# Kernel tuning notes

Hardware: AMD Instinct MI355X
Metric: run time of the kernel (lower is better)

The kernel has to match this reference:

```python
import jax, jax.numpy as jnp
import numpy as np

N = 50000
E = 800000
D_IN = 128
H = 128
K = 64
BN_EPS = 1e-5


def setup_inputs() -> dict:
    key = jax.random.key(0)
    ks = jax.random.split(key, 16)
    s_in = 1.0 / np.sqrt(D_IN)
    s_h = 1.0 / np.sqrt(H)
    inp = {
        "x": jax.random.normal(ks[0], (N, D_IN), dtype=jnp.float32),
        "edge_index": jax.random.randint(ks[1], (2, E), 0, N, dtype=jnp.int64),
        # GIN layer 1 MLP (Linear(D_IN,H) -> ReLU -> Linear(H,H)), eps1, BN1
        "W1a": jax.random.uniform(ks[2], (D_IN, H), jnp.float32, -s_in, s_in),
        "b1a": jnp.zeros((H,), jnp.float32),
        "W1b": jax.random.uniform(ks[3], (H, H), jnp.float32, -s_h, s_h),
        "b1b": jnp.zeros((H,), jnp.float32),
        "eps1": jnp.zeros((), jnp.float32),
        "gamma1": jnp.ones((H,), jnp.float32),
        "beta1": jnp.zeros((H,), jnp.float32),
        # GIN layer 2 MLP, eps2, BN2
        "W2a": jax.random.uniform(ks[4], (H, H), jnp.float32, -s_h, s_h),
        "b2a": jnp.zeros((H,), jnp.float32),
        "W2b": jax.random.uniform(ks[5], (H, H), jnp.float32, -s_h, s_h),
        "b2b": jnp.zeros((H,), jnp.float32),
        "eps2": jnp.zeros((), jnp.float32),
        "gamma2": jnp.ones((H,), jnp.float32),
        "beta2": jnp.zeros((H,), jnp.float32),
        # final projection (no bias) and learnable log temperature
        "Wout": jax.random.uniform(ks[6], (H, K), jnp.float32, -s_h, s_h),
        "log_tau": jnp.zeros((), jnp.float32),  # log(1.0)
    }
    return inp


def _gin_layer(x, src, dst, Wa, ba, Wb, bb, eps):
    # GINConv: mlp((1+eps)*x + sum_{j in N(i)} x_j), scatter-add over edges
    agg = jax.ops.segment_sum(x[src], dst, num_segments=N)  # [N, d]
    h = (1.0 + eps) * x + agg
    h = jax.nn.relu(h @ Wa + ba) @ Wb + bb
    return h


def _batchnorm(x, gamma, beta):
    # training-mode BatchNorm1d over node dim (biased variance)
    m = jnp.mean(x, axis=0)
    v = jnp.mean(jnp.square(x - m), axis=0)
    return (x - m) * jax.lax.rsqrt(v + BN_EPS) * gamma + beta


def reference(x, edge_index, W1a, b1a, W1b, b1b, eps1, gamma1, beta1,
              W2a, b2a, W2b, b2b, eps2, gamma2, beta2, Wout, log_tau):
    src, dst = edge_index[0], edge_index[1]
    h = _gin_layer(x, src, dst, W1a, b1a, W1b, b1b, eps1)
    h = jax.nn.relu(_batchnorm(h, gamma1, beta1))
    h = _gin_layer(h, src, dst, W2a, b2a, W2b, b2b, eps2)
    h = jax.nn.relu(_batchnorm(h, gamma2, beta2))
    logits = h @ Wout  # [N, K]
    tau = jnp.exp(log_tau)
    S = jax.nn.softmax(logits / tau, axis=-1)
    return (S, logits)
```

## Files before the change

### kernel.cpp

```cpp
#include <hip/hip_runtime.h>
#include <hip/hip_fp16.h>


#define NNODES 50000
#define NEDGES 800000
#define HD 128
#define KOUT 64
#define NCLS 8
#define CLSW 6250
#define HIST_BLKS 512

typedef __attribute__((ext_vector_type(8))) _Float16 f16x8;
typedef __attribute__((ext_vector_type(4))) float f32x4;

__device__ __forceinline__ unsigned short f2h_bits(float f) {
    _Float16 h = (_Float16)f;
    return __builtin_bit_cast(unsigned short, h);
}
__device__ __forceinline__ f16x8 h8_relu(f16x8 v) {
    #pragma unroll
    for (int i = 0; i < 8; ++i) v[i] = (v[i] > (_Float16)0.f) ? v[i] : (_Float16)0.f;
    return v;
}

__global__ __launch_bounds__(256) void prep_all(
    const float* __restrict__ x, unsigned short* __restrict__ xh,
    const float* __restrict__ W1a, const float* __restrict__ W1b,
    const float* __restrict__ W2a, const float* __restrict__ W2b,
    unsigned short* __restrict__ wt1a, unsigned short* __restrict__ wt1b,
    unsigned short* __restrict__ wt2a, unsigned short* __restrict__ wt2b,
    const int* __restrict__ ei, int* __restrict__ deg)
{
    __shared__ int h[CLSW];
    int bid = blockIdx.x;
    if (bid < HIST_BLKS) {
        const int cls = bid & 7;
        const int lo = cls * CLSW;
        const int e0 = (bid >> 3) * 12500;
        for (int i = threadIdx.x; i < CLSW; i += 256) h[i] = 0;
        __syncthreads();
        for (int e = e0 + threadIdx.x; e < e0 + 12500; e += 256) {
            unsigned d = (unsigned)(ei[NEDGES + e] - lo);
            if (d < (unsigned)CLSW) atomicAdd(&h[d], 1);
        }
        __syncthreads();
        for (int i = threadIdx.x; i < CLSW; i += 256) {
            int v = h[i];
            if (v) atomicAdd(&deg[lo + i], v);
        }
    } else if (bid < HIST_BLKS + 6250) {
        int i = (bid - HIST_BLKS) * 256 + threadIdx.x;
        float4 v = ((const float4*)x)[i];
        ushort4 o;
        o.x = f2h_bits(v.x); o.y = f2h_bits(v.y);
        o.z = f2h_bits(v.z); o.w = f2h_bits(v.w);
        ((ushort4*)xh)[i] = o;
    } else {
        int wb = bid - (HIST_BLKS + 6250);
        int w = wb >> 6;
        int idx = (wb & 63) * 256 + threadIdx.x;
        int n = idx >> 7, k = idx & 127;
        const float* W = (w == 0) ? W1a : (w == 1) ? W1b : (w == 2) ? W2a : W2b;
        unsigned short* Wt = (w == 0) ? wt1a : (w == 1) ? wt1b : (w == 2) ? wt2a : wt2b;
        Wt[idx] = f2h_bits(W[k * HD + n]);
    }
}

__global__ __launch_bounds__(256) void scan_a(
    const int* __restrict__ deg, int* __restrict__ incl, int* __restrict__ bsum)
{
    __shared__ int s[256];
    int t = threadIdx.x, idx = blockIdx.x * 256 + t;
    int v = (idx < NNODES) ? deg[idx] : 0;
    s[t] = v; __syncthreads();
    #pragma unroll
    for (int off = 1; off < 256; off <<= 1) {
        int tmp = (t >= off) ? s[t - off] : 0;
        __syncthreads();
        s[t] += tmp;
        __syncthreads();
    }
    if (idx < NNODES) incl[idx] = s[t];
    if (t == 255) bsum[blockIdx.x] = s[255];
}

__global__ __launch_bounds__(256) void scan_b(
    const int* __restrict__ bsum, int* __restrict__ bscan, int nblk)
{
    __shared__ int s[256];
    int t = threadIdx.x;
    s[t] = (t < nblk) ? bsum[t] : 0; __syncthreads();
    #pragma unroll
    for (int off = 1; off < 256; off <<= 1) {
        int tmp = (t >= off) ? s[t - off] : 0;
        __syncthreads();
        s[t] += tmp;
        __syncthreads();
    }
    bscan[t] = s[t];
}

__global__ __launch_bounds__(256) void scan_c(
    const int* __restrict__ deg, const int* __restrict__ incl,
    const int* __restrict__ bscan,
    int* __restrict__ row_start, int* __restrict__ cur)
{
    int b = blockIdx.x, t = threadIdx.x, idx = b * 256 + t;
    if (idx >= NNODES) return;
    int off = (b > 0) ? bscan[b - 1] : 0;
    int ex = incl[idx] - deg[idx] + off;
    row_start[idx] = ex;
    cur[idx] = ex;
}

__global__ __launch_bounds__(256) void edge_fill(
    const int* __restrict__ ei, int* __restrict__ cur, int* __restrict__ col)
{
    const int cls = blockIdx.x & 7;
    const int e0 = (blockIdx.x >> 3) * 3125;
    for (int e = e0 + threadIdx.x; e < e0 + 3125; e += 256) {
        int dst = ei[NEDGES + e];
        if (dst / CLSW == cls) {
            int pos = atomicAdd(&cur[dst], 1);
            col[pos] = ei[e];
        }
    }
}

template<bool BN>
__global__ __launch_bounds__(256) void gin_gather_w(
    const unsigned short* __restrict__ Xh, const int* __restrict__ col,
    const int* __restrict__ rs, const int* __restrict__ re,
    const float* __restrict__ eps,
    const float* __restrict__ scale, const float* __restrict__ shift,
    unsigned short* __restrict__ H0h)
{
    const int t = threadIdx.x;
    const int g = t >> 4;
    const int lane = t & 15;
    const f16x8* X8 = (const f16x8*)Xh;
    const float alphaf = 1.f + eps[0];

    f16x8 sc8, sh8, al8;
    #pragma unroll
    for (int i = 0; i < 8; ++i) al8[i] = (_Float16)alphaf;
    if (BN) {
        #pragma unroll
        for (int i = 0; i < 8; ++i) {
            sc8[i] = (_Float16)scale[lane * 8 + i];
            sh8[i] = (_Float16)shift[lane * 8 + i];
        }
    }

    #pragma unroll 1
    for (int nn = 0; nn < 2; ++nn) {
        int node = blockIdx.x * 32 + nn * 16 + g;
        if (node >= NNODES) continue;

        f16x8 acc = X8[(long)node * 16 + lane];
        if (BN) acc = h8_relu(acc * sc8 + sh8);
        acc = acc * al8;

        int j = rs[node], end = re[node];
        for (; j + 3 < end; j += 4) {
            f16x8 u0 = X8[(long)col[j]     * 16 + lane];
            f16x8 u1 = X8[(long)col[j + 1] * 16 + lane];
            f16x8 u2 = X8[(long)col[j + 2] * 16 + lane];
            f16x8 u3 = X8[(long)col[j + 3] * 16 + lane];
            if (BN) {
                u0 = h8_relu(u0 * sc8 + sh8);
                u1 = h8_relu(u1 * sc8 + sh8);
                u2 = h8_relu(u2 * sc8 + sh8);
                u3 = h8_relu(u3 * sc8 + sh8);
            }
            acc += (u0 + u1) + (u2 + u3);
        }
        for (; j < end; ++j) {
            f16x8 u = X8[(long)col[j] * 16 + lane];
            if (BN) u = h8_relu(u * sc8 + sh8);
            acc += u;
        }

        ((f16x8*)H0h)[(long)node * 16 + lane] = acc;
    }
}

__global__ __launch_bounds__(256) void mlp_mfma(
    const unsigned short* __restrict__ A,
    const unsigned short* __restrict__ Wta,
    const float* __restrict__ biasa,
    const unsigned short* __restrict__ Wtb,
    const float* __restrict__ biasb,
    unsigned short* __restrict__ Cb,
    float* __restrict__ Cf,
    float* __restrict__ out_sum, float* __restrict__ out_sq)
{
    __shared__ _Float16 Wsa[128][136];
    __shared__ _Float16 Wsb[128][136];
    float (*Cs)[132] = (float(*)[132]) & Wsa[0][0];
    float* redp = (float*)&Wsb[0][0];

    const int t = threadIdx.x;
    const int wave = t >> 6, lane = t & 63;
    const int m16 = lane & 15, quad = lane >> 4;
    const int row0 = blockIdx.x * 64;
    const int arow = row0 + wave * 16 + m16;

    #pragma unroll
    for (int i = 0; i < 8; ++i) {
        int idx = t + i * 256;
        int r = idx >> 4, s = idx & 15;
        *(float4*)&Wsa[r][s * 8] = ((const float4*)Wta)[idx];
        *(float4*)&Wsb[r][s * 8] = ((const float4*)Wtb)[idx];
    }

    f16x8 afrag[4];
    if (arow < NNODES) {
        const _Float16* ar = (const _Float16*)A + (long)arow * HD + quad * 8;
        #pragma unroll
        for (int kc = 0; kc < 4; ++kc)
            afrag[kc] = *(const f16x8*)(ar + kc * 32);
    } else {
        #pragma unroll
        for (int kc = 0; kc < 4; ++kc)
            afrag[kc] = f16x8{0, 0, 0, 0, 0, 0, 0, 0};
    }
    __syncthreads();

    f32x4 accs[8];
    #pragma unroll
    for (int np = 0; np < 8; np += 2) {
        f32x4 a0 = {0.f, 0.f, 0.f, 0.f};
        f32x4 a1 = {0.f, 0.f, 0.f, 0.f};
        const _Float16* b0 = &Wsa[np * 16 + m16][quad * 8];
        const _Float16* b1 = &Wsa[(np + 1) * 16 + m16][quad * 8];
        #pragma unroll
        for (int kc = 0; kc < 4; ++kc) {
            f16x8 f0 = *(const f16x8*)(b0 + kc * 32);
            f16x8 f1 = *(const f16x8*)(b1 + kc * 32);
            a0 = __builtin_amdgcn_mfma_f32_16x16x32_f16(afrag[kc], f0, a0, 0, 0, 0);
            a1 = __builtin_amdgcn_mfma_f32_16x16x32_f16(afrag[kc], f1, a1, 0, 0, 0);
        }
        accs[np] = a0; accs[np + 1] = a1;
    }
    __syncthreads();

    #pragma unroll
    for (int np = 0; np < 8; ++np) {
        int c = np * 16 + m16;
        float bb = biasa[c];
        #pragma unroll
        for (int r = 0; r < 4; ++r)
            Cs[wave * 16 + quad * 4 + r][c] = fmaxf(accs[np][r] + bb, 0.f);
    }
    __syncthreads();

    f16x8 afrag2[4];
    {
        const int crow = wave * 16 + m16;
        #pragma unroll
        for (int kc = 0; kc < 4; ++kc) {
            const float* cp = &Cs[crow][quad * 8 + kc * 32];
            float4 c0 = *(const float4*)cp;
            float4 c1 = *(const float4*)(cp + 4);
            f16x8 fr;
            fr[0] = (_Float16)c0.x; fr[1] = (_Float16)c0.y;
            fr[2] = (_Float16)c0.z; fr[3] = (_Float16)c0.w;
            fr[4] = (_Float16)c1.x; fr[5] = (_Float16)c1.y;
            fr[6] = (_Float16)c1.z; fr[7] = (_Float16)c1.w;
            afrag2[kc] = fr;
        }
    }
    #pragma unroll
    for (int np = 0; np < 8; np += 2) {
        f32x4 a0 = {0.f, 0.f, 0.f, 0.f};
        f32x4 a1 = {0.f, 0.f, 0.f, 0.f};
        const _Float16* b0 = &Wsb[np * 16 + m16][quad * 8];
        const _Float16* b1 = &Wsb[(np + 1) * 16 + m16][quad * 8];
        #pragma unroll
        for (int kc = 0; kc < 4; ++kc) {
            f16x8 f0 = *(const f16x8*)(b0 + kc * 32);
            f16x8 f1 = *(const f16x8*)(b1 + kc * 32);
            a0 = __builtin_amdgcn_mfma_f32_16x16x32_f16(afrag2[kc], f0, a0, 0, 0, 0);
            a1 = __builtin_amdgcn_mfma_f32_16x16x32_f16(afrag2[kc], f1, a1, 0, 0, 0);
        }
        accs[np] = a0; accs[np + 1] = a1;
    }
    __syncthreads();

    #pragma unroll
    for (int np = 0; np < 8; ++np) {
        int c = np * 16 + m16;
        float bb = biasb[c];
        #pragma unroll
        for (int r = 0; r < 4; ++r)
            Cs[wave * 16 + quad * 4 + r][c] = accs[np][r] + bb;
    }
    __syncthreads();

    const int s4 = t & 31;
    const int rb = t >> 5;
    float lsum[4] = {}, lsq[4] = {};
    #pragma unroll
    for (int i = 0; i < 8; ++i) {
        int r = rb + i * 8;
        int row = row0 + r;
        float4 v = *(const float4*)&Cs[r][s4 * 4];
        if (row < NNODES) {
            if (Cb) {
                ushort4 o;
                o.x = f2h_bits(v.x); o.y = f2h_bits(v.y);
                o.z = f2h_bits(v.z); o.w = f2h_bits(v.w);
                ((ushort4*)Cb)[(long)row * 32 + s4] = o;
            }
            if (Cf) ((float4*)Cf)[(long)row * 32 + s4] = v;
            lsum[0] += v.x; lsum[1] += v.y; lsum[2] += v.z; lsum[3] += v.w;
            lsq[0] = fmaf(v.x, v.x, lsq[0]);
            lsq[1] = fmaf(v.y, v.y, lsq[1]);
            lsq[2] = fmaf(v.z, v.z, lsq[2]);
            lsq[3] = fmaf(v.w, v.w, lsq[3]);
        }
    }
    #pragma unroll
    for (int j = 0; j < 4; ++j) {
        redp[(0 * 8 + rb) * 128 + s4 * 4 + j] = lsum[j];
        redp[(1 * 8 + rb) * 128 + s4 * 4 + j] = lsq[j];
    }
    __syncthreads();
    if (t < 128) {
        float s = 0.f, q = 0.f;
        #pragma unroll
        for (int g = 0; g < 8; ++g) {
            s += redp[g * 128 + t];
            q += redp[(8 + g) * 128 + t];
        }
        atomicAdd(&out_sum[t], s);
        atomicAdd(&out_sq[t],  q);
    }
}

__global__ void bn_prep(const float* __restrict__ ssum, const float* __restrict__ ssq,
                        const float* __restrict__ gamma, const float* __restrict__ beta,
                        float* __restrict__ scale, float* __restrict__ shift)
{
    int c = threadIdx.x;
    const float invN = 1.0f / (float)NNODES;
    float m = ssum[c] * invN;
    float var = fmaf(-m, m, ssq[c] * invN);
    float rs = rsqrtf(var + 1e-5f);
    float sc = gamma[c] * rs;
    scale[c] = sc;
    shift[c] = beta[c] - m * sc;
}

__global__ __launch_bounds__(256) void out_proj_softmax(
    const float* __restrict__ H, const float* __restrict__ Wout,
    const float* __restrict__ scale, const float* __restrict__ shift,
    const float* __restrict__ log_tau,
    float* __restrict__ outS, float* __restrict__ outL)
{
    __shared__ float As[HD][20];
    const int t = threadIdx.x;
    const long row0 = (long)blockIdx.x * 16;

    #pragma unroll
    for (int i = 0; i < 8; ++i) {
        int idx = t + i * 256;
        int r = idx >> 7, cc = idx & 127;
        float v = H[(row0 + r) * HD + cc];
        As[cc][r] = fmaxf(fmaf(v, scale[cc], shift[cc]), 0.f);
    }
    __syncthreads();

    const int c = t & 63;
    const int g = t >> 6;
    float acc[4] = {};

    float wq[8];
    #pragma unroll
    for (int i = 0; i < 8; ++i) wq[i] = Wout[i * KOUT + c];

    #pragma unroll 1
    for (int kc = 0; kc < HD; kc += 8) {
        float wn[8];
        if (kc + 8 < HD) {
            #pragma unroll
            for (int i = 0; i < 8; ++i) wn[i] = Wout[(kc + 8 + i) * KOUT + c];
        }
        #pragma unroll
        for (int i = 0; i < 8; ++i) {
            float4 a = *(const float4*)&As[kc + i][g * 4];
            acc[0] = fmaf(a.x, wq[i], acc[0]);
            acc[1] = fmaf(a.y, wq[i], acc[1]);
            acc[2] = fmaf(a.z, wq[i], acc[2]);
            acc[3] = fmaf(a.w, wq[i], acc[3]);
        }
        if (kc + 8 < HD) {
            #pragma unroll
            for (int i = 0; i < 8; ++i) wq[i] = wn[i];
        }
    }

    float inv_tau = __expf(-log_tau[0]);
    #pragma unroll
    for (int i = 0; i < 4; ++i) {
        float z = acc[i] * inv_tau;
        float m = z;
        #pragma unroll
        for (int o = 32; o > 0; o >>= 1) m = fmaxf(m, __shfl_xor(m, o));
        float e = __expf(z - m);
        float s = e;
        #pragma unroll
        for (int o = 32; o > 0; o >>= 1) s += __shfl_xor(s, o);
        long oi = (row0 + g * 4 + i) * KOUT + c;
        outS[oi] = e / s;
        outL[oi] = acc[i];
    }
}

extern "C" void kernel_launch(void* const* d_in, const int* in_sizes, int n_in,
                              void* d_out, int out_size, void* d_ws, size_t ws_size,
                              hipStream_t stream)
{
    const float* x      = (const float*)d_in[0];
    const int*   ei     = (const int*)d_in[1];
    const float* W1a    = (const float*)d_in[2];
    const float* b1a    = (const float*)d_in[3];
    const float* W1b    = (const float*)d_in[4];
    const float* b1b    = (const float*)d_in[5];
    const float* eps1   = (const float*)d_in[6];
    const float* gamma1 = (const float*)d_in[7];
    const float* beta1  = (const float*)d_in[8];
    const float* W2a    = (const float*)d_in[9];
    const float* b2a    = (const float*)d_in[10];
    const float* W2b    = (const float*)d_in[11];
    const float* b2b    = (const float*)d_in[12];
    const float* eps2   = (const float*)d_in[13];
    const float* gamma2 = (const float*)d_in[14];
    const float* beta2  = (const float*)d_in[15];
    const float* Wout   = (const float*)d_in[16];
    const float* ltau   = (const float*)d_in[17];

    const size_t NB = (size_t)NNODES * HD;
    float* B0 = (float*)d_ws;
    float* B1 = B0 + NB;
    float* B2 = B1 + NB;
    float* ST = B2 + NB;
    float* sum1 = ST, *sq1 = ST + 128, *sum2 = ST + 256, *sq2 = ST + 384;
    float* scale1 = ST + 512, *shift1 = ST + 640, *scale2 = ST + 768, *shift2 = ST + 896;

    unsigned short* xh  = (unsigned short*)B2;
    unsigned short* h0h = (unsigned short*)B0;
    unsigned short* hh  = (unsigned short*)B0;
    unsigned short* h2h = (unsigned short*)B2;

    int* I0        = (int*)(ST + 1024);
    int* deg       = I0;
    int* incl      = I0 + 50048;
    int* row_start = I0 + 2 * 50048;
    int* cur       = I0 + 3 * 50048;
    int* bsum      = I0 + 4 * 50048;
    int* bscan     = bsum + 256;
    int* col       = bscan + 256;
    unsigned short* wt1a = (unsigned short*)(col + NEDGES);
    unsigned short* wt1b = wt1a + HD * HD;
    unsigned short* wt2a = wt1b + HD * HD;
    unsigned short* wt2b = wt2a + HD * HD;

    const int SCAN_BLKS = (NNODES + 255) / 256;
    const int GEMM_BLKS = (NNODES + 63) / 64;
    const int GATH_BLKS = (NNODES + 31) / 32;

    hipMemsetAsync(ST, 0, 512 * sizeof(float), stream);
    hipMemsetAsync(deg, 0, NNODES * sizeof(int), stream);
    prep_all<<<HIST_BLKS + 6506, 256, 0, stream>>>(x, xh, W1a, W1b, W2a, W2b,
                                                   wt1a, wt1b, wt2a, wt2b, ei, deg);
    scan_a<<<SCAN_BLKS, 256, 0, stream>>>(deg, incl, bsum);
    scan_b<<<1, 256, 0, stream>>>(bsum, bscan, SCAN_BLKS);
    scan_c<<<SCAN_BLKS, 256, 0, stream>>>(deg, incl, bscan, row_start, cur);
    edge_fill<<<2048, 256, 0, stream>>>(ei, cur, col);

    gin_gather_w<false><<<GATH_BLKS, 256, 0, stream>>>(
        xh, col, row_start, cur, eps1, nullptr, nullptr, h0h);
    mlp_mfma<<<GEMM_BLKS, 256, 0, stream>>>(
        h0h, wt1a, b1a, wt1b, b1b, hh, nullptr, sum1, sq1);
    bn_prep<<<1, 128, 0, stream>>>(sum1, sq1, gamma1, beta1, scale1, shift1);

    gin_gather_w<true><<<GATH_BLKS, 256, 0, stream>>>(
        hh, col, row_start, cur, eps2, scale1, shift1, h2h);
    mlp_mfma<<<GEMM_BLKS, 256, 0, stream>>>(
        h2h, wt2a, b2a, wt2b, b2b, nullptr, B1, sum2, sq2);
    bn_prep<<<1, 128, 0, stream>>>(sum2, sq2, gamma2, beta2, scale2, shift2);

    out_proj_softmax<<<NNODES / 16, 256, 0, stream>>>(
        B1, Wout, scale2, shift2, ltau,
        (float*)d_out, (float*)d_out + (size_t)NNODES * KOUT);
}
```

Measured before the change: 328.5 us.

## Fold BN stat finalization into consumer kernels and shrink MLP shared memory

Removes the two single-block bn_prep launches by having each block of the BN gather and output-projection kernels compute scale and shift from the accumulated sums into shared memory. Separately, mlp_mfma now reuses one weight buffer for both layers: the second weight matrix is staged in registers and written to LDS after the first GEMM, and the intermediate activation is kept as fp16. This cuts LDS use from about 70KB to 52KB to raise occupancy, at the cost of redundant per-block BN math and higher register pressure.

```diff
diff --git a/kernel.cpp b/kernel.cpp
--- a/kernel.cpp
+++ b/kernel.cpp
@@ -132,23 +132,38 @@
     const unsigned short* __restrict__ Xh, const int* __restrict__ col,
     const int* __restrict__ rs, const int* __restrict__ re,
     const float* __restrict__ eps,
-    const float* __restrict__ scale, const float* __restrict__ shift,
+    const float* __restrict__ ssum, const float* __restrict__ ssq,
+    const float* __restrict__ gamma, const float* __restrict__ beta,
     unsigned short* __restrict__ H0h)
 {
+    __shared__ float s_sc[128], s_sh[128];
     const int t = threadIdx.x;
     const int g = t >> 4;
     const int lane = t & 15;
     const f16x8* X8 = (const f16x8*)Xh;
     const float alphaf = 1.f + eps[0];
 
+    if (BN) {
+        if (t < 128) {
+            const float invN = 1.0f / (float)NNODES;
+            float m = ssum[t] * invN;
+            float var = fmaf(-m, m, ssq[t] * invN);
+            float rsq = rsqrtf(var + 1e-5f);
+            float sc = gamma[t] * rsq;
+            s_sc[t] = sc;
+            s_sh[t] = fmaf(-m, sc, beta[t]);
+        }
+        __syncthreads();
+    }
+
     f16x8 sc8, sh8, al8;
     #pragma unroll
     for (int i = 0; i < 8; ++i) al8[i] = (_Float16)alphaf;
     if (BN) {
         #pragma unroll
         for (int i = 0; i < 8; ++i) {
-            sc8[i] = (_Float16)scale[lane * 8 + i];
-            sh8[i] = (_Float16)shift[lane * 8 + i];
+            sc8[i] = (_Float16)s_sc[lane * 8 + i];
+            sh8[i] = (_Float16)s_sh[lane * 8 + i];
         }
     }
 
@@ -195,10 +210,12 @@
     float* __restrict__ Cf,
     float* __restrict__ out_sum, float* __restrict__ out_sq)
 {
-    __shared__ _Float16 Wsa[128][136];
-    __shared__ _Float16 Wsb[128][136];
-    float (*Cs)[132] = (float(*)[132]) & Wsa[0][0];
-    float* redp = (float*)&Wsb[0][0];
+    __shared__ float4 smem4[(34816 + 17408) / 16];
+    char* smem = (char*)smem4;
+    _Float16 (*Wbuf)[136] = (_Float16(*)[136])smem;
+    _Float16 (*Cs16)[136] = (_Float16(*)[136])(smem + 34816);
+    float (*CsF)[132] = (float(*)[132])smem;
+    float* redp = (float*)(smem + 34816);
 
     const int t = threadIdx.x;
     const int wave = t >> 6, lane = t & 63;
@@ -206,12 +223,13 @@
     const int row0 = blockIdx.x * 64;
     const int arow = row0 + wave * 16 + m16;
 
+    float4 wreg[8];
     #pragma unroll
     for (int i = 0; i < 8; ++i) {
         int idx = t + i * 256;
         int r = idx >> 4, s = idx & 15;
-        *(float4*)&Wsa[r][s * 8] = ((const float4*)Wta)[idx];
-        *(float4*)&Wsb[r][s * 8] = ((const float4*)Wtb)[idx];
+        *(float4*)&Wbuf[r][s * 8] = ((const float4*)Wta)[idx];
+        wreg[i] = ((const float4*)Wtb)[idx];
     }
 
     f16x8 afrag[4];
@@ -232,8 +250,8 @@
     for (int np = 0; np < 8; np += 2) {
         f32x4 a0 = {0.f, 0.f, 0.f, 0.f};
         f32x4 a1 = {0.f, 0.f, 0.f, 0.f};
-        const _Float16* b0 = &Wsa[np * 16 + m16][quad * 8];
-        const _Float16* b1 = &Wsa[(np + 1) * 16 + m16][quad * 8];
+        const _Float16* b0 = &Wbuf[np * 16 + m16][quad * 8];
+        const _Float16* b1 = &Wbuf[(np + 1) * 16 + m16][quad * 8];
         #pragma unroll
         for (int kc = 0; kc < 4; ++kc) {
             f16x8 f0 = *(const f16x8*)(b0 + kc * 32);
@@ -246,12 +264,19 @@
     __syncthreads();
 
     #pragma unroll
+    for (int i = 0; i < 8; ++i) {
+        int idx = t + i * 256;
+        int r = idx >> 4, s = idx & 15;
+        *(float4*)&Wbuf[r][s * 8] = wreg[i];
+    }
+    #pragma unroll
     for (int np = 0; np < 8; ++np) {
         int c = np * 16 + m16;
         float bb = biasa[c];
         #pragma unroll
         for (int r = 0; r < 4; ++r)
-            Cs[wave * 16 + quad * 4 + r][c] = fmaxf(accs[np][r] + bb, 0.f);
+            Cs16[wave * 16 + quad * 4 + r][c] =
+                (_Float16)fmaxf(accs[np][r] + bb, 0.f);
     }
     __syncthreads();
 
@@ -259,24 +284,15 @@
     {
         const int crow = wave * 16 + m16;
         #pragma unroll
-        for (int kc = 0; kc < 4; ++kc) {
-            const float* cp = &Cs[crow][quad * 8 + kc * 32];
-            float4 c0 = *(const float4*)cp;
-            float4 c1 = *(const float4*)(cp + 4);
-            f16x8 fr;
-            fr[0] = (_Float16)c0.x; fr[1] = (_Float16)c0.y;
-            fr[2] = (_Float16)c0.z; fr[3] = (_Float16)c0.w;
-            fr[4] = (_Float16)c1.x; fr[5] = (_Float16)c1.y;
-            fr[6] = (_Float16)c1.z; fr[7] = (_Float16)c1.w;
-            afrag2[kc] = fr;
-        }
+        for (int kc = 0; kc < 4; ++kc)
+            afrag2[kc] = *(const f16x8*)&Cs16[crow][quad * 8 + kc * 32];
     }
     #pragma unroll
     for (int np = 0; np < 8; np += 2) {
         f32x4 a0 = {0.f, 0.f, 0.f, 0.f};
         f32x4 a1 = {0.f, 0.f, 0.f, 0.f};
-        const _Float16* b0 = &Wsb[np * 16 + m16][quad * 8];
-        const _Float16* b1 = &Wsb[(np + 1) * 16 + m16][quad * 8];
+        const _Float16* b0 = &Wbuf[np * 16 + m16][quad * 8];
+        const _Float16* b1 = &Wbuf[(np + 1) * 16 + m16][quad * 8];
         #pragma unroll
         for (int kc = 0; kc < 4; ++kc) {
             f16x8 f0 = *(const f16x8*)(b0 + kc * 32);
@@ -294,7 +310,7 @@
         float bb = biasb[c];
         #pragma unroll
         for (int r = 0; r < 4; ++r)
-            Cs[wave * 16 + quad * 4 + r][c] = accs[np][r] + bb;
+            CsF[wave * 16 + quad * 4 + r][c] = accs[np][r] + bb;
     }
     __syncthreads();
 
@@ -305,7 +321,7 @@
     for (int i = 0; i < 8; ++i) {
         int r = rb + i * 8;
         int row = row0 + r;
-        float4 v = *(const float4*)&Cs[r][s4 * 4];
+        float4 v = *(const float4*)&CsF[r][s4 * 4];
         if (row < NNODES) {
             if (Cb) {
                 ushort4 o;
@@ -339,36 +355,35 @@
     }
 }
 
-__global__ void bn_prep(const float* __restrict__ ssum, const float* __restrict__ ssq,
-                        const float* __restrict__ gamma, const float* __restrict__ beta,
-                        float* __restrict__ scale, float* __restrict__ shift)
-{
-    int c = threadIdx.x;
-    const float invN = 1.0f / (float)NNODES;
-    float m = ssum[c] * invN;
-    float var = fmaf(-m, m, ssq[c] * invN);
-    float rs = rsqrtf(var + 1e-5f);
-    float sc = gamma[c] * rs;
-    scale[c] = sc;
-    shift[c] = beta[c] - m * sc;
-}
-
 __global__ __launch_bounds__(256) void out_proj_softmax(
     const float* __restrict__ H, const float* __restrict__ Wout,
-    const float* __restrict__ scale, const float* __restrict__ shift,
+    const float* __restrict__ ssum, const float* __restrict__ ssq,
+    const float* __restrict__ gamma, const float* __restrict__ beta,
     const float* __restrict__ log_tau,
     float* __restrict__ outS, float* __restrict__ outL)
 {
     __shared__ float As[HD][20];
+    __shared__ float s_sc[128], s_sh[128];
     const int t = threadIdx.x;
     const long row0 = (long)blockIdx.x * 16;
+
+    if (t < 128) {
+        const float invN = 1.0f / (float)NNODES;
+        float m = ssum[t] * invN;
+        float var = fmaf(-m, m, ssq[t] * invN);
+        float rsq = rsqrtf(var + 1e-5f);
+        float sc = gamma[t] * rsq;
+        s_sc[t] = sc;
+        s_sh[t] = fmaf(-m, sc, beta[t]);
+    }
+    __syncthreads();
 
     #pragma unroll
     for (int i = 0; i < 8; ++i) {
         int idx = t + i * 256;
         int r = idx >> 7, cc = idx & 127;
         float v = H[(row0 + r) * HD + cc];
-        As[cc][r] = fmaxf(fmaf(v, scale[cc], shift[cc]), 0.f);
+        As[cc][r] = fmaxf(fmaf(v, s_sc[cc], s_sh[cc]), 0.f);
     }
     __syncthreads();
 
@@ -447,7 +462,6 @@
     float* B2 = B1 + NB;
     float* ST = B2 + NB;
     float* sum1 = ST, *sq1 = ST + 128, *sum2 = ST + 256, *sq2 = ST + 384;
-    float* scale1 = ST + 512, *shift1 = ST + 640, *scale2 = ST + 768, *shift2 = ST + 896;
 
     unsigned short* xh  = (unsigned short*)B2;
     unsigned short* h0h = (unsigned short*)B0;
@@ -481,18 +495,16 @@
     edge_fill<<<2048, 256, 0, stream>>>(ei, cur, col);
 
     gin_gather_w<false><<<GATH_BLKS, 256, 0, stream>>>(
-        xh, col, row_start, cur, eps1, nullptr, nullptr, h0h);
+        xh, col, row_start, cur, eps1, nullptr, nullptr, nullptr, nullptr, h0h);
     mlp_mfma<<<GEMM_BLKS, 256, 0, stream>>>(
         h0h, wt1a, b1a, wt1b, b1b, hh, nullptr, sum1, sq1);
-    bn_prep<<<1, 128, 0, stream>>>(sum1, sq1, gamma1, beta1, scale1, shift1);
 
     gin_gather_w<true><<<GATH_BLKS, 256, 0, stream>>>(
-        hh, col, row_start, cur, eps2, scale1, shift1, h2h);
+        hh, col, row_start, cur, eps2, sum1, sq1, gamma1, beta1, h2h);
     mlp_mfma<<<GEMM_BLKS, 256, 0, stream>>>(
         h2h, wt2a, b2a, wt2b, b2b, nullptr, B1, sum2, sq2);
-    bn_prep<<<1, 128, 0, stream>>>(sum2, sq2, gamma2, beta2, scale2, shift2);
 
     out_proj_softmax<<<NNODES / 16, 256, 0, stream>>>(
-        B1, Wout, scale2, shift2, ltau,
+        B1, Wout, sum2, sq2, gamma2, beta2, ltau,
         (float*)d_out, (float*)d_out + (size_t)NNODES * KOUT);
 }
```

After: 333.8 us. About the same (+1.6%).
